# Kernel optimization log

Hardware: AMD Instinct MI355X
Metric: run time of the kernel (lower is better)

## Reference

```python
import jax, jax.numpy as jnp
import numpy as np

N_NODES = 50000
N_EDGES = 800000
B, W, D, OUT = 2, 128, 64, 128


def setup_inputs() -> dict:
    key = jax.random.key(0)
    ks = jax.random.split(key, 8)
    s = lambda k, shape, fan: jax.random.normal(k, shape, dtype=jnp.float32) / np.sqrt(fan)
    return {
        "x": jax.random.normal(ks[0], (B, N_NODES, W), dtype=jnp.float32),
        "embeddings": jax.random.normal(ks[1], (N_NODES, D), dtype=jnp.float32),
        "edge_index": jax.random.randint(ks[2], (2, N_EDGES), 0, N_NODES, dtype=jnp.int64),
        "Wq": s(ks[3], (D, D), D),
        "Wk": s(ks[4], (D, D), D),
        "v": s(ks[5], (D,), D),
        "fcW": s(ks[6], (OUT, 2 * W), 2 * W),
        "fcb": jnp.zeros((OUT,), dtype=jnp.float32),
    }


def reference(x, embeddings, edge_index, Wq, Wk, v, fcW, fcb):
    B_, N, W_ = x.shape
    src, dst = edge_index[0], edge_index[1]

    # Project once on nodes, then gather per edge (same math as gather-then-linear).
    e_q = embeddings @ Wq.T        # [N, D]
    e_k = embeddings @ Wk.T        # [N, D]
    score = jnp.tanh(e_q[src] + e_k[dst]) @ v   # [E]

    # Scatter-softmax over destination nodes.
    max_vals = jax.ops.segment_max(score, dst, num_segments=N)   # [N], -inf for empty
    exp_src = jnp.exp(score - max_vals[dst])                     # [E]
    sum_exp = jax.ops.segment_sum(exp_src, dst, num_segments=N)  # [N]
    attn = exp_src / (sum_exp[dst] + 1e-8)                       # [E]

    # Weighted scatter-add aggregation of source features.
    weighted = x[:, src, :] * attn[None, :, None]                # [B, E, W]
    agg = jax.ops.segment_sum(jnp.swapaxes(weighted, 0, 1), dst, num_segments=N)  # [N, B, W]
    agg = jnp.swapaxes(agg, 0, 1)                                # [B, N, W]

    out = jnp.concatenate([x, agg], axis=-1) @ fcW.T + fcb       # [B, N, OUT]
    return jax.nn.relu(out)
```

## Files before the change

### kernel.cpp

```cpp
#include <hip/hip_runtime.h>
#include <hip/hip_bf16.h>
#include <math.h>

#define N_NODES 50000
#define N_EDGES 800000
#define BB 2
#define WFEAT 128
#define DD 64
#define OUTD 128
#define NROWS (BB * N_NODES)
#define SCAN_B 256
#define NBLK ((N_NODES + SCAN_B - 1) / SCAN_B)

#define PROJ_TB ((N_NODES + 127) / 128)
#define CVTX_B 6250
#define CVTW_B 16
#define HIST_B 3125
#define TRIPLE_B (3 * HIST_B)
#define PREP_B (TRIPLE_B + CVTW_B)
#define PS_B (PROJ_TB + NBLK)

typedef __attribute__((ext_vector_type(8))) short bf16x8;
typedef __attribute__((ext_vector_type(4))) float f32x4;
typedef __attribute__((ext_vector_type(2))) float f32x2;
typedef __attribute__((ext_vector_type(8))) unsigned short ushort8;

#define PRESCALE 2.8853900817779268f
#define L2E 1.4426950408889634f

static __device__ __forceinline__ unsigned short f2bf(float f) {
    __hip_bfloat16 h = __float2bfloat16(f);
    return *reinterpret_cast<unsigned short*>(&h);
}
static __device__ __forceinline__ float bf_lo(unsigned int w) {
    return __uint_as_float(w << 16);
}
static __device__ __forceinline__ float bf_hi(unsigned int w) {
    return __uint_as_float(w & 0xFFFF0000u);
}
static __device__ __forceinline__ float exp2_hw(float x) {
    float r;
    asm("v_exp_f32 %0, %1" : "=v"(r) : "v"(x));
    return r;
}
template <int CTRL>
static __device__ __forceinline__ float ror_add(float x) {
    int xi = __float_as_int(x);
    int r = __builtin_amdgcn_update_dpp(xi, xi, CTRL, 0xF, 0xF, true);
    return x + __int_as_float(r);
}
static __device__ __forceinline__ float row_reduce(float x) {
    x = ror_add<0x128>(x);
    x = ror_add<0x124>(x);
    x = ror_add<0x122>(x);
    x = ror_add<0x121>(x);
    return x;
}

__global__ __launch_bounds__(256) void prep_kernel(const float* __restrict__ x,
                                                   unsigned short* __restrict__ xb2,
                                                   unsigned char* __restrict__ xf8,
                                                   const float* __restrict__ fcW,
                                                   unsigned short* __restrict__ fcWb,
                                                   const int* __restrict__ dstp,
                                                   int* __restrict__ deg,
                                                   unsigned short* __restrict__ posin) {
    int bid = blockIdx.x;
    int tid = threadIdx.x;
    if (bid < TRIPLE_B) {
        int q = bid / 3;
        int r = bid - q * 3;
        if (r < 2) {
            int t = (q * 2 + r) * 256 + tid;
            const float4* in4 = (const float4*)x;
            float4 a = in4[2 * t], b = in4[2 * t + 1];
            ushort8 o;
            o[0] = f2bf(a.x); o[1] = f2bf(a.y); o[2] = f2bf(a.z); o[3] = f2bf(a.w);
            o[4] = f2bf(b.x); o[5] = f2bf(b.y); o[6] = f2bf(b.z); o[7] = f2bf(b.w);
            int f0 = t * 8;
            int bb = f0 >= N_NODES * WFEAT;
            int rem = f0 - bb * (N_NODES * WFEAT);
            int node = rem >> 7, feat = rem & 127;
            *reinterpret_cast<ushort8*>(&xb2[(size_t)node * 256 + bb * 128 + feat]) = o;
            int w0 = __builtin_amdgcn_cvt_pk_fp8_f32(a.x, a.y, 0, false);
            w0     = __builtin_amdgcn_cvt_pk_fp8_f32(a.z, a.w, w0, true);
            int w1 = __builtin_amdgcn_cvt_pk_fp8_f32(b.x, b.y, 0, false);
            w1     = __builtin_amdgcn_cvt_pk_fp8_f32(b.z, b.w, w1, true);
            uint2 pk; pk.x = (unsigned int)w0; pk.y = (unsigned int)w1;
            *reinterpret_cast<uint2*>(&xf8[(size_t)node * 256 + bb * 128 + feat]) = pk;
        } else {
            int e = q * 256 + tid;
            int d = dstp[e];
            posin[e] = (unsigned short)atomicAdd(&deg[d], 1);
        }
    } else {
        int t = (bid - TRIPLE_B) * 256 + tid;
        const float4* in4 = (const float4*)fcW;
        float4 a = in4[2 * t], b = in4[2 * t + 1];
        ushort8 o;
        o[0] = f2bf(a.x); o[1] = f2bf(a.y); o[2] = f2bf(a.z); o[3] = f2bf(a.w);
        o[4] = f2bf(b.x); o[5] = f2bf(b.y); o[6] = f2bf(b.z); o[7] = f2bf(b.w);
        *reinterpret_cast<ushort8*>(&fcWb[8 * t]) = o;
    }
}

__global__ __launch_bounds__(256) void proj_scan(const float* __restrict__ emb,
                                                 const float* __restrict__ Wq,
                                                 const float* __restrict__ Wk,
                                                 unsigned short* __restrict__ eqb,
                                                 unsigned short* __restrict__ ekb,
                                                 const int* __restrict__ deg,
                                                 int* __restrict__ bsum) {
    __shared__ unsigned short As[128 * 64];
    __shared__ unsigned short Bs[128 * 64];
    int tid = threadIdx.x;
    if (blockIdx.x >= PROJ_TB) {
        int* sh = (int*)As;
        int i = (blockIdx.x - PROJ_TB) * SCAN_B + tid;
        sh[tid] = (i < N_NODES) ? deg[i] : 0;
        __syncthreads();
        for (int s = SCAN_B / 2; s; s >>= 1) {
            if (tid < s) sh[tid] += sh[tid + s];
            __syncthreads();
        }
        if (tid == 0) bsum[blockIdx.x - PROJ_TB] = sh[0];
        return;
    }
    int wave = tid >> 6, lane = tid & 63;
    int wm = wave >> 1, wn = wave & 1;
    int row0 = blockIdx.x * 128;

#pragma unroll
    for (int c = 0; c < 4; ++c) {
        int idx = (c * 256 + tid) * 8;
        int r = idx >> 6, k = idx & 63;
        int byte = (r * 128 + k * 2) ^ ((r & 7) << 4);

        int node = row0 + r;
        ushort8 o = {};
        if (node < N_NODES) {
            const float4* p = (const float4*)(emb + (size_t)node * DD + k);
            float4 a = p[0], b = p[1];
            o[0] = f2bf(a.x); o[1] = f2bf(a.y); o[2] = f2bf(a.z); o[3] = f2bf(a.w);
            o[4] = f2bf(b.x); o[5] = f2bf(b.y); o[6] = f2bf(b.z); o[7] = f2bf(b.w);
        }
        *reinterpret_cast<ushort8*>(reinterpret_cast<char*>(As) + byte) = o;

        const float* wsrc = (r < 64) ? (Wq + r * DD + k) : (Wk + (r - 64) * DD + k);
        float4 wa = *(const float4*)wsrc, wb = *((const float4*)wsrc + 1);
        ushort8 ow;
        ow[0] = f2bf(wa.x); ow[1] = f2bf(wa.y); ow[2] = f2bf(wa.z); ow[3] = f2bf(wa.w);
        ow[4] = f2bf(wb.x); ow[5] = f2bf(wb.y); ow[6] = f2bf(wb.z); ow[7] = f2bf(wb.w);
        *reinterpret_cast<ushort8*>(reinterpret_cast<char*>(Bs) + byte) = ow;
    }
    __syncthreads();

    f32x4 acc[4][4] = {};
#pragma unroll
    for (int kk = 0; kk < 2; ++kk) {
        bf16x8 a[4], b[4];
#pragma unroll
        for (int m = 0; m < 4; ++m) {
            int r = wm * 64 + m * 16 + (lane & 15);
            int k = kk * 32 + (lane >> 4) * 8;
            int byte = (r * 128 + k * 2) ^ ((r & 7) << 4);
            a[m] = *reinterpret_cast<bf16x8*>(reinterpret_cast<char*>(As) + byte);
        }
#pragma unroll
        for (int n = 0; n < 4; ++n) {
            int cn = wn * 64 + n * 16 + (lane & 15);
            int k = kk * 32 + (lane >> 4) * 8;
            int byte = (cn * 128 + k * 2) ^ ((cn & 7) << 4);
            b[n] = *reinterpret_cast<bf16x8*>(reinterpret_cast<char*>(Bs) + byte);
        }
#pragma unroll
        for (int m = 0; m < 4; ++m)
#pragma unroll
            for (int n = 0; n < 4; ++n)
                acc[m][n] = __builtin_amdgcn_mfma_f32_16x16x32_bf16(a[m], b[n], acc[m][n], 0, 0, 0);
    }

#pragma unroll
    for (int m = 0; m < 4; ++m) {
#pragma unroll
        for (int n = 0; n < 4; ++n) {
            int col = wn * 64 + n * 16 + (lane & 15);
#pragma unroll
            for (int j = 0; j < 4; ++j) {
                int row = row0 + wm * 64 + m * 16 + (lane >> 4) * 4 + j;
                if (row < N_NODES) {
                    unsigned short val = f2bf(PRESCALE * acc[m][n][j]);
                    if (col < 64) eqb[(size_t)row * DD + col] = val;
                    else          ekb[(size_t)row * DD + col - 64] = val;
                }
            }
        }
    }
}

__global__ void scan_final(const int* __restrict__ deg, const int* __restrict__ bsum,
                           int* __restrict__ rowptr) {
    __shared__ int shb[SCAN_B];
    __shared__ int sh[SCAN_B];
    int tid = threadIdx.x;
    int bv = (tid < NBLK) ? bsum[tid] : 0;
    shb[tid] = bv;
    __syncthreads();
    for (int s = 1; s < SCAN_B; s <<= 1) {
        int t = (tid >= s) ? shb[tid - s] : 0;
        __syncthreads();
        shb[tid] += t;
        __syncthreads();
    }
    int myprefix = (blockIdx.x == 0) ? 0 : shb[blockIdx.x - 1];

    int i = blockIdx.x * SCAN_B + tid;
    int v = (i < N_NODES) ? deg[i] : 0;
    sh[tid] = v;
    __syncthreads();
    for (int s = 1; s < SCAN_B; s <<= 1) {
        int t = 0;
        if (tid >= s) t = sh[tid - s];
        __syncthreads();
        sh[tid] += t;
        __syncthreads();
    }
    if (i < N_NODES) {
        int excl = sh[tid] - v + myprefix;
        rowptr[i] = excl;
        if (i == N_NODES - 1) rowptr[N_NODES] = excl + v;
    }
}

__global__ void scatter_kernel(const int* __restrict__ src, const int* __restrict__ dst,
                               const int* __restrict__ rowptr,
                               const unsigned short* __restrict__ posin,
                               int* __restrict__ src_sorted) {
    int t = blockIdx.x * blockDim.x + threadIdx.x;
    if (t < 12) src_sorted[N_EDGES + t] = 0;
    int e4 = t * 4;
    if (e4 + 3 < N_EDGES) {
        int4 d4 = *reinterpret_cast<const int4*>(dst + e4);
        ushort4 p4 = *reinterpret_cast<const ushort4*>(posin + e4);
        int4 s4 = *reinterpret_cast<const int4*>(src + e4);
        src_sorted[rowptr[d4.x] + p4.x] = s4.x;
        src_sorted[rowptr[d4.y] + p4.y] = s4.y;
        src_sorted[rowptr[d4.z] + p4.z] = s4.z;
        src_sorted[rowptr[d4.w] + p4.w] = s4.w;
    } else {
        for (int e = e4; e < N_EDGES; ++e)
            src_sorted[rowptr[dst[e]] + posin[e]] = src[e];
    }
}

__global__ __launch_bounds__(256) void agg_fused(const unsigned short* __restrict__ eqb,
                                                 const unsigned short* __restrict__ ekb,
                                                 const float* __restrict__ v,
                                                 const unsigned char* __restrict__ xf8,
                                                 const int* __restrict__ rowptr,
                                                 const int* __restrict__ src_sorted,
                                                 unsigned short* __restrict__ aggb2) {
    int node = (blockIdx.x * 256 + threadIdx.x) >> 6;
    if (node >= N_NODES) return;
    int lane = threadIdx.x & 63;
    int g = lane >> 4, hl = lane & 15;

    uint2 eku = *reinterpret_cast<const uint2*>(ekb + (size_t)node * DD + 4 * hl);
    float k0 = bf_lo(eku.x), k1 = bf_hi(eku.x), k2 = bf_lo(eku.y), k3 = bf_hi(eku.y);
    float4 vv = *reinterpret_cast<const float4*>(v + 4 * hl);
    float vs = row_reduce(vv.x + vv.y + vv.z + vv.w);
    float vtotl2 = vs * L2E;

    int beg = rowptr[node], end = rowptr[node + 1];
    int nIter = (end - beg + 3) >> 2;

    float sum = 0.f;
    f32x2 a0[4] = {}, a1[4] = {};

    int s_cur = src_sorted[beg + g];
    int s_nxt = src_sorted[beg + 4 + g];
    uint2 equ = *reinterpret_cast<const uint2*>(eqb + (size_t)s_cur * DD + 4 * hl);
    const unsigned char* xr = xf8 + (size_t)s_cur * 256 + 8 * hl;
    uint2 u0 = *reinterpret_cast<const uint2*>(xr);
    uint2 u1 = *reinterpret_cast<const uint2*>(xr + 128);

    for (int i = 0; i < nIter; ++i) {
        bool valid = (beg + 4 * i + g) < end;
        int s_n2 = src_sorted[beg + 4 * (i + 2) + g];
        uint2 equn = *reinterpret_cast<const uint2*>(eqb + (size_t)s_nxt * DD + 4 * hl);
        const unsigned char* xrn = xf8 + (size_t)s_nxt * 256 + 8 * hl;
        uint2 u0n = *reinterpret_cast<const uint2*>(xrn);
        uint2 u1n = *reinterpret_cast<const uint2*>(xrn + 128);

        float s0 = bf_lo(equ.x) + k0, s1 = bf_hi(equ.x) + k1;
        float s2 = bf_lo(equ.y) + k2, s3 = bf_hi(equ.y) + k3;
        float r =      vv.x * __builtin_amdgcn_rcpf(exp2_hw(s0) + 1.f);
        r = fmaf(vv.y, __builtin_amdgcn_rcpf(exp2_hw(s1) + 1.f), r);
        r = fmaf(vv.z, __builtin_amdgcn_rcpf(exp2_hw(s2) + 1.f), r);
        r = fmaf(vv.w, __builtin_amdgcn_rcpf(exp2_hw(s3) + 1.f), r);
        r = row_reduce(r);
        float w = exp2_hw(fmaf(-2.f * L2E, r, vtotl2));
        w = valid ? w : 0.f;
        sum += w;

        f32x2 p;
        p = __builtin_amdgcn_cvt_pk_f32_fp8((int)u0.x, false); a0[0] += w * p;
        p = __builtin_amdgcn_cvt_pk_f32_fp8((int)u0.x, true);  a0[1] += w * p;
        p = __builtin_amdgcn_cvt_pk_f32_fp8((int)u0.y, false); a0[2] += w * p;
        p = __builtin_amdgcn_cvt_pk_f32_fp8((int)u0.y, true);  a0[3] += w * p;
        p = __builtin_amdgcn_cvt_pk_f32_fp8((int)u1.x, false); a1[0] += w * p;
        p = __builtin_amdgcn_cvt_pk_f32_fp8((int)u1.x, true);  a1[1] += w * p;
        p = __builtin_amdgcn_cvt_pk_f32_fp8((int)u1.y, false); a1[2] += w * p;
        p = __builtin_amdgcn_cvt_pk_f32_fp8((int)u1.y, true);  a1[3] += w * p;

        equ = equn; u0 = u0n; u1 = u1n;
        s_nxt = s_n2;
    }

    sum += __shfl_xor(sum, 16); sum += __shfl_xor(sum, 32);
#pragma unroll
    for (int j = 0; j < 4; ++j) {
        a0[j].x += __shfl_xor(a0[j].x, 16); a0[j].x += __shfl_xor(a0[j].x, 32);
        a0[j].y += __shfl_xor(a0[j].y, 16); a0[j].y += __shfl_xor(a0[j].y, 32);
        a1[j].x += __shfl_xor(a1[j].x, 16); a1[j].x += __shfl_xor(a1[j].x, 32);
        a1[j].y += __shfl_xor(a1[j].y, 16); a1[j].y += __shfl_xor(a1[j].y, 32);
    }
    float inv = __builtin_amdgcn_rcpf(sum + 1e-8f);

    if (g < 2) {
        float c0 = (g ? a1[0].x : a0[0].x) * inv, c1 = (g ? a1[0].y : a0[0].y) * inv;
        float c2 = (g ? a1[1].x : a0[1].x) * inv, c3 = (g ? a1[1].y : a0[1].y) * inv;
        float c4 = (g ? a1[2].x : a0[2].x) * inv, c5 = (g ? a1[2].y : a0[2].y) * inv;
        float c6 = (g ? a1[3].x : a0[3].x) * inv, c7 = (g ? a1[3].y : a0[3].y) * inv;
        uint4 o;
        o.x = (unsigned int)f2bf(c0) | ((unsigned int)f2bf(c1) << 16);
        o.y = (unsigned int)f2bf(c2) | ((unsigned int)f2bf(c3) << 16);
        o.z = (unsigned int)f2bf(c4) | ((unsigned int)f2bf(c5) << 16);
        o.w = (unsigned int)f2bf(c6) | ((unsigned int)f2bf(c7) << 16);
        *reinterpret_cast<uint4*>(&aggb2[(size_t)node * 256 + (size_t)g * 128 + 8 * hl]) = o;
    }
}

__global__ __launch_bounds__(256) void fc_mfma(const unsigned short* __restrict__ xb2,
                                               const unsigned short* __restrict__ aggb2,
                                               const unsigned short* __restrict__ fcWb,
                                               const float* __restrict__ fcb,
                                               float* __restrict__ out) {
    __shared__ unsigned short As[128 * 64];
    __shared__ unsigned short Bs[128 * 64];
    int tid = threadIdx.x;
    int wave = tid >> 6, lane = tid & 63;
    int wm = wave >> 1, wn = wave & 1;
    int row0 = blockIdx.x * 128;

    f32x4 acc[4][4] = {};

    for (int ks = 0; ks < 4; ++ks) {
        const unsigned short* Asrc = (ks < 2) ? xb2 : aggb2;
        int kbase = (ks & 1) * 64;
        __syncthreads();
#pragma unroll
        for (int c = 0; c < 4; ++c) {
            int idx = (c * 256 + tid) * 8;
            int r = idx >> 6, k = idx & 63;
            int row = row0 + r;
            ulonglong2 val = make_ulonglong2(0ull, 0ull);
            if (row < NROWS) {
                int batch = row >= N_NODES;
                int nd = row - (batch ? N_NODES : 0);
                val = *reinterpret_cast<const ulonglong2*>(
                        &Asrc[(size_t)nd * 256 + batch * 128 + kbase + k]);
            }
            int byte = (r * 128 + k * 2) ^ ((r & 7) << 4);
            *reinterpret_cast<ulonglong2*>(reinterpret_cast<char*>(As) + byte) = val;

            ulonglong2 wv = *reinterpret_cast<const ulonglong2*>(&fcWb[(size_t)r * 256 + ks * 64 + k]);
            *reinterpret_cast<ulonglong2*>(reinterpret_cast<char*>(Bs) + byte) = wv;
        }
        __syncthreads();
#pragma unroll
        for (int kk = 0; kk < 2; ++kk) {
            bf16x8 a[4], b[4];
#pragma unroll
            for (int m = 0; m < 4; ++m) {
                int r = wm * 64 + m * 16 + (lane & 15);
                int k = kk * 32 + (lane >> 4) * 8;
                int byte = (r * 128 + k * 2) ^ ((r & 7) << 4);
                a[m] = *reinterpret_cast<bf16x8*>(reinterpret_cast<char*>(As) + byte);
            }
#pragma unroll
            for (int n = 0; n < 4; ++n) {
                int cn = wn * 64 + n * 16 + (lane & 15);
                int k = kk * 32 + (lane >> 4) * 8;
                int byte = (cn * 128 + k * 2) ^ ((cn & 7) << 4);
                b[n] = *reinterpret_cast<bf16x8*>(reinterpret_cast<char*>(Bs) + byte);
            }
#pragma unroll
            for (int m = 0; m < 4; ++m)
#pragma unroll
                for (int n = 0; n < 4; ++n)
                    acc[m][n] = __builtin_amdgcn_mfma_f32_16x16x32_bf16(a[m], b[n], acc[m][n], 0, 0, 0);
        }
    }
#pragma unroll
    for (int m = 0; m < 4; ++m) {
#pragma unroll
        for (int n = 0; n < 4; ++n) {
            int col = wn * 64 + n * 16 + (lane & 15);
            float bias = fcb[col];
#pragma unroll
            for (int j = 0; j < 4; ++j) {
                int row = row0 + wm * 64 + m * 16 + (lane >> 4) * 4 + j;
                if (row < NROWS)
                    out[(size_t)row * OUTD + col] = fmaxf(acc[m][n][j] + bias, 0.f);
            }
        }
    }
}

extern "C" void kernel_launch(void* const* d_in, const int* in_sizes, int n_in,
                              void* d_out, int out_size, void* d_ws, size_t ws_size,
                              hipStream_t stream) {
    const float* x    = (const float*)d_in[0];
    const float* emb  = (const float*)d_in[1];
    const int*   eidx = (const int*)d_in[2];
    const float* Wq   = (const float*)d_in[3];
    const float* Wk   = (const float*)d_in[4];
    const float* v    = (const float*)d_in[5];
    const float* fcW  = (const float*)d_in[6];
    const float* fcb  = (const float*)d_in[7];
    float* out = (float*)d_out;

    char* ws = (char*)d_ws;
    unsigned short* eqb  = (unsigned short*)ws;                  ws += (size_t)N_NODES * DD * 2;
    unsigned short* ekb  = (unsigned short*)ws;                  ws += (size_t)N_NODES * DD * 2;
    unsigned short* xb2  = (unsigned short*)ws;                  ws += (size_t)NROWS * WFEAT * 2;
    unsigned char*  xf8  = (unsigned char*)ws;                   ws += (size_t)NROWS * WFEAT;
    unsigned short* aggb2= (unsigned short*)ws;                  ws += (size_t)NROWS * WFEAT * 2;
    unsigned short* fcWb = (unsigned short*)ws;                  ws += (size_t)OUTD * 256 * 2;
    int* deg        = (int*)ws;                                  ws += (size_t)N_NODES * 4;
    int* rowptr     = (int*)ws;                                  ws += (size_t)(N_NODES + 1) * 4 + 12;
    unsigned short* posin = (unsigned short*)ws;                 ws += (size_t)N_EDGES * 2;
    int* bsum       = (int*)ws;                                  ws += 256 * 4;
    int* src_sorted = (int*)ws;

    const int* srcp = eidx;
    const int* dstp = eidx + N_EDGES;

    hipMemsetAsync(deg, 0, (size_t)N_NODES * sizeof(int), stream);

    prep_kernel<<<PREP_B, 256, 0, stream>>>(x, xb2, xf8, fcW, fcWb, dstp, deg, posin);
    proj_scan<<<PS_B, 256, 0, stream>>>(emb, Wq, Wk, eqb, ekb, deg, bsum);
    scan_final<<<NBLK, SCAN_B, 0, stream>>>(deg, bsum, rowptr);
    scatter_kernel<<<(N_EDGES / 4 + 255) / 256, 256, 0, stream>>>(srcp, dstp, rowptr, posin,
                                                                  src_sorted);
    agg_fused<<<(N_NODES * 64 + 255) / 256, 256, 0, stream>>>(eqb, ekb, v, xf8, rowptr,
                                                              src_sorted, aggb2);
    fc_mfma<<<(NROWS + 127) / 128, 256, 0, stream>>>(xb2, aggb2, fcWb, fcb, out);
}
```

Baseline: 153.6 us.

## Interleave per-node e_q and fp8 features into one 384-byte gather record

Packs each source node's bf16 e_q projection (128 B) and both batches' fp8 features (256 B) into a single contiguous 384-byte record. The edge-gather loop in the aggregation kernel then reads e_q and features from one address per edge, which touches fewer separate cache lines and DRAM pages. It also rewrites the tanh-score arithmetic using packed float2 vector operations, which may map onto packed FP32 instructions. The record stride of 384 bytes is not a power of two, and the address is computed in 32-bit unsigned arithmetic.

```diff
diff --git a/kernel.cpp b/kernel.cpp
--- a/kernel.cpp
+++ b/kernel.cpp
@@ -20,6 +20,8 @@
 #define PREP_B (TRIPLE_B + CVTW_B)
 #define PS_B (PROJ_TB + NBLK)
 
+#define RECB 384
+
 typedef __attribute__((ext_vector_type(8))) short bf16x8;
 typedef __attribute__((ext_vector_type(4))) float f32x4;
 typedef __attribute__((ext_vector_type(2))) float f32x2;
@@ -59,7 +61,7 @@
 
 __global__ __launch_bounds__(256) void prep_kernel(const float* __restrict__ x,
                                                    unsigned short* __restrict__ xb2,
-                                                   unsigned char* __restrict__ xf8,
+                                                   unsigned char* __restrict__ nrec,
                                                    const float* __restrict__ fcW,
                                                    unsigned short* __restrict__ fcWb,
                                                    const int* __restrict__ dstp,
@@ -87,7 +89,7 @@
             int w1 = __builtin_amdgcn_cvt_pk_fp8_f32(b.x, b.y, 0, false);
             w1     = __builtin_amdgcn_cvt_pk_fp8_f32(b.z, b.w, w1, true);
             uint2 pk; pk.x = (unsigned int)w0; pk.y = (unsigned int)w1;
-            *reinterpret_cast<uint2*>(&xf8[(size_t)node * 256 + bb * 128 + feat]) = pk;
+            *reinterpret_cast<uint2*>(&nrec[(size_t)node * RECB + 128 + bb * 128 + feat]) = pk;
         } else {
             int e = q * 256 + tid;
             int d = dstp[e];
@@ -107,7 +109,7 @@
 __global__ __launch_bounds__(256) void proj_scan(const float* __restrict__ emb,
                                                  const float* __restrict__ Wq,
                                                  const float* __restrict__ Wk,
-                                                 unsigned short* __restrict__ eqb,
+                                                 unsigned char* __restrict__ nrec,
                                                  unsigned short* __restrict__ ekb,
                                                  const int* __restrict__ deg,
                                                  int* __restrict__ bsum) {
@@ -190,8 +192,10 @@
                 int row = row0 + wm * 64 + m * 16 + (lane >> 4) * 4 + j;
                 if (row < N_NODES) {
                     unsigned short val = f2bf(PRESCALE * acc[m][n][j]);
-                    if (col < 64) eqb[(size_t)row * DD + col] = val;
-                    else          ekb[(size_t)row * DD + col - 64] = val;
+                    if (col < 64)
+                        *reinterpret_cast<unsigned short*>(&nrec[(size_t)row * RECB + col * 2]) = val;
+                    else
+                        ekb[(size_t)row * DD + col - 64] = val;
                 }
             }
         }
@@ -253,10 +257,9 @@
     }
 }
 
-__global__ __launch_bounds__(256) void agg_fused(const unsigned short* __restrict__ eqb,
+__global__ __launch_bounds__(256) void agg_fused(const unsigned char* __restrict__ nrec,
                                                  const unsigned short* __restrict__ ekb,
                                                  const float* __restrict__ v,
-                                                 const unsigned char* __restrict__ xf8,
                                                  const int* __restrict__ rowptr,
                                                  const int* __restrict__ src_sorted,
                                                  unsigned short* __restrict__ aggb2) {
@@ -266,10 +269,15 @@
     int g = lane >> 4, hl = lane & 15;
 
     uint2 eku = *reinterpret_cast<const uint2*>(ekb + (size_t)node * DD + 4 * hl);
-    float k0 = bf_lo(eku.x), k1 = bf_hi(eku.x), k2 = bf_lo(eku.y), k3 = bf_hi(eku.y);
+    f32x2 kk01, kk23;
+    kk01.x = bf_lo(eku.x); kk01.y = bf_hi(eku.x);
+    kk23.x = bf_lo(eku.y); kk23.y = bf_hi(eku.y);
     float4 vv = *reinterpret_cast<const float4*>(v + 4 * hl);
+    f32x2 vv01, vv23;
+    vv01.x = vv.x; vv01.y = vv.y; vv23.x = vv.z; vv23.y = vv.w;
     float vs = row_reduce(vv.x + vv.y + vv.z + vv.w);
     float vtotl2 = vs * L2E;
+    f32x2 one2; one2.x = 1.f; one2.y = 1.f;
 
     int beg = rowptr[node], end = rowptr[node + 1];
     int nIter = (end - beg + 3) >> 2;
@@ -279,26 +287,33 @@
 
     int s_cur = src_sorted[beg + g];
     int s_nxt = src_sorted[beg + 4 + g];
-    uint2 equ = *reinterpret_cast<const uint2*>(eqb + (size_t)s_cur * DD + 4 * hl);
-    const unsigned char* xr = xf8 + (size_t)s_cur * 256 + 8 * hl;
-    uint2 u0 = *reinterpret_cast<const uint2*>(xr);
-    uint2 u1 = *reinterpret_cast<const uint2*>(xr + 128);
+    const unsigned char* rec = nrec + (unsigned int)(s_cur * RECB + 8 * hl);
+    uint2 equ = *reinterpret_cast<const uint2*>(rec);
+    uint2 u0 = *reinterpret_cast<const uint2*>(rec + 128);
+    uint2 u1 = *reinterpret_cast<const uint2*>(rec + 256);
 
     for (int i = 0; i < nIter; ++i) {
         bool valid = (beg + 4 * i + g) < end;
         int s_n2 = src_sorted[beg + 4 * (i + 2) + g];
-        uint2 equn = *reinterpret_cast<const uint2*>(eqb + (size_t)s_nxt * DD + 4 * hl);
-        const unsigned char* xrn = xf8 + (size_t)s_nxt * 256 + 8 * hl;
-        uint2 u0n = *reinterpret_cast<const uint2*>(xrn);
-        uint2 u1n = *reinterpret_cast<const uint2*>(xrn + 128);
-
-        float s0 = bf_lo(equ.x) + k0, s1 = bf_hi(equ.x) + k1;
-        float s2 = bf_lo(equ.y) + k2, s3 = bf_hi(equ.y) + k3;
-        float r =      vv.x * __builtin_amdgcn_rcpf(exp2_hw(s0) + 1.f);
-        r = fmaf(vv.y, __builtin_amdgcn_rcpf(exp2_hw(s1) + 1.f), r);
-        r = fmaf(vv.z, __builtin_amdgcn_rcpf(exp2_hw(s2) + 1.f), r);
-        r = fmaf(vv.w, __builtin_amdgcn_rcpf(exp2_hw(s3) + 1.f), r);
-        r = row_reduce(r);
+        const unsigned char* recn = nrec + (unsigned int)(s_nxt * RECB + 8 * hl);
+        uint2 equn = *reinterpret_cast<const uint2*>(recn);
+        uint2 u0n = *reinterpret_cast<const uint2*>(recn + 128);
+        uint2 u1n = *reinterpret_cast<const uint2*>(recn + 256);
+
+        f32x2 q01, q23;
+        q01.x = bf_lo(equ.x); q01.y = bf_hi(equ.x);
+        q23.x = bf_lo(equ.y); q23.y = bf_hi(equ.y);
+        q01 += kk01; q23 += kk23;
+        f32x2 ex01, ex23;
+        ex01.x = exp2_hw(q01.x); ex01.y = exp2_hw(q01.y);
+        ex23.x = exp2_hw(q23.x); ex23.y = exp2_hw(q23.y);
+        ex01 += one2; ex23 += one2;
+        f32x2 rc;
+        rc.x = __builtin_amdgcn_rcpf(ex01.x); rc.y = __builtin_amdgcn_rcpf(ex01.y);
+        f32x2 r2 = vv01 * rc;
+        rc.x = __builtin_amdgcn_rcpf(ex23.x); rc.y = __builtin_amdgcn_rcpf(ex23.y);
+        r2 += vv23 * rc;
+        float r = row_reduce(r2.x + r2.y);
         float w = exp2_hw(fmaf(-2.f * L2E, r, vtotl2));
         w = valid ? w : 0.f;
         sum += w;
@@ -432,10 +447,9 @@
     float* out = (float*)d_out;
 
     char* ws = (char*)d_ws;
-    unsigned short* eqb  = (unsigned short*)ws;                  ws += (size_t)N_NODES * DD * 2;
+    unsigned char*  nrec = (unsigned char*)ws;                   ws += (size_t)N_NODES * RECB;
     unsigned short* ekb  = (unsigned short*)ws;                  ws += (size_t)N_NODES * DD * 2;
     unsigned short* xb2  = (unsigned short*)ws;                  ws += (size_t)NROWS * WFEAT * 2;
-    unsigned char*  xf8  = (unsigned char*)ws;                   ws += (size_t)NROWS * WFEAT;
     unsigned short* aggb2= (unsigned short*)ws;                  ws += (size_t)NROWS * WFEAT * 2;
     unsigned short* fcWb = (unsigned short*)ws;                  ws += (size_t)OUTD * 256 * 2;
     int* deg        = (int*)ws;                                  ws += (size_t)N_NODES * 4;
@@ -449,12 +463,12 @@
 
     hipMemsetAsync(deg, 0, (size_t)N_NODES * sizeof(int), stream);
 
-    prep_kernel<<<PREP_B, 256, 0, stream>>>(x, xb2, xf8, fcW, fcWb, dstp, deg, posin);
-    proj_scan<<<PS_B, 256, 0, stream>>>(emb, Wq, Wk, eqb, ekb, deg, bsum);
+    prep_kernel<<<PREP_B, 256, 0, stream>>>(x, xb2, nrec, fcW, fcWb, dstp, deg, posin);
+    proj_scan<<<PS_B, 256, 0, stream>>>(emb, Wq, Wk, nrec, ekb, deg, bsum);
     scan_final<<<NBLK, SCAN_B, 0, stream>>>(deg, bsum, rowptr);
     scatter_kernel<<<(N_EDGES / 4 + 255) / 256, 256, 0, stream>>>(srcp, dstp, rowptr, posin,
                                                                   src_sorted);
-    agg_fused<<<(N_NODES * 64 + 255) / 256, 256, 0, stream>>>(eqb, ekb, v, xf8, rowptr,
+    agg_fused<<<(N_NODES * 64 + 255) / 256, 256, 0, stream>>>(nrec, ekb, v, rowptr,
                                                               src_sorted, aggb2);
     fc_mfma<<<(NROWS + 127) / 128, 256, 0, stream>>>(xb2, aggb2, fcWb, fcb, out);
 }
```

Result: no change. 154.3 us, median of 2 (+0.5%).
